# Optimization experiments

Hardware: AMD Instinct MI355X
Metric: run time of the kernel (lower is better)

Reference implementation:

```python
import jax, jax.numpy as jnp
import numpy as np

MAX_SEQ_LEN = 4096

def bigbird_block_rand_mask(from_seq_length, to_seq_length, from_block_size, to_block_size, num_rand_blocks, last_idx=-1):
    rand_attn = np.zeros((from_seq_length // from_block_size - 2, num_rand_blocks), dtype=np.int32)
    middle_seq = np.arange(1, to_seq_length // to_block_size - 1, dtype=np.int32)
    last = to_seq_length // to_block_size - 1
    if last_idx > 2 * to_block_size:
        last = last_idx // to_block_size - 1
    r = num_rand_blocks
    nfb = from_seq_length // from_block_size
    for i in range(1, nfb - 1):
        start = i - 2
        end = i
        if i == 1:
            rand_attn[i - 1, :] = np.random.permutation(middle_seq[2:last])[:r]
        elif i == 2:
            rand_attn[i - 1, :] = np.random.permutation(middle_seq[3:last])[:r]
        elif i == nfb - 3:
            rand_attn[i - 1, :] = np.random.permutation(middle_seq[:last])[:r]
        elif i == nfb - 2:
            rand_attn[i - 1, :] = np.random.permutation(middle_seq[:last])[:r]
        elif start > last:
            start = last
            rand_attn[i - 1, :] = np.random.permutation(middle_seq[:start])[:r]
        elif end + 1 == last:
            rand_attn[i - 1, :] = np.random.permutation(middle_seq[:start])[:r]
        else:
            rand_attn[i - 1, :] = np.random.permutation(np.concatenate((middle_seq[:start], middle_seq[end + 1:last])))[:r]
    return rand_attn

def full_bigbird_mask(from_seq_length, to_seq_length, from_block_size, to_block_size, rand_attn):
    attn_mask = np.zeros((MAX_SEQ_LEN, MAX_SEQ_LEN), dtype=np.int32)
    for i in range(1, from_seq_length // from_block_size - 1):
        attn_mask[i * from_block_size:(i + 1) * from_block_size, (i - 1) * to_block_size:(i + 2) * to_block_size] = 1
        for j in rand_attn[i - 1, :]:
            attn_mask[i * from_block_size:(i + 1) * from_block_size, j * to_block_size:(j + 1) * to_block_size] = 1
    attn_mask[:from_block_size, :] = 1
    attn_mask[:, :to_block_size] = 1
    attn_mask[:, -to_block_size:] = 1
    attn_mask[-from_block_size:, :] = 1
    return attn_mask[:from_seq_length, :to_seq_length].astype(bool)

def setup_inputs() -> dict:
    B, H, F, T, D = 2, 16, 1024, 1024, 64
    BS, R, SEED = 64, 3, 0
    np.random.seed(SEED)
    rand_attn = np.stack([
        bigbird_block_rand_mask(MAX_SEQ_LEN, MAX_SEQ_LEN, BS, BS, R, last_idx=1024)[:F // BS - 2]
        for _ in range(H)
    ], axis=0)
    mask = np.stack([full_bigbird_mask(F, T, BS, BS, rand_attn[h]) for h in range(H)], axis=0)
    attention_mask = jnp.asarray(mask[None].astype(np.float32))  # [1, H, F, T]
    key = jax.random.key(0)
    kq, kk, kv = jax.random.split(key, 3)
    return {
        'query_layer': jax.random.normal(kq, (B, H, F, D), dtype=jnp.float32),
        'key_layer': jax.random.normal(kk, (B, H, T, D), dtype=jnp.float32),
        'value_layer': jax.random.normal(kv, (B, H, T, D), dtype=jnp.float32),
        'attention_mask': attention_mask,
    }

def reference(query_layer, key_layer, value_layer, attention_mask):
    d = query_layer.shape[-1]
    scores = jnp.einsum('bnfh,bnth->bnft', query_layer, key_layer) * (1.0 / np.sqrt(float(d)))
    scores = scores + (1.0 - attention_mask) * -10000.0
    probs = jax.nn.softmax(scores, axis=-1)
    # [batch, from_seq, heads, size_per_head]
    return jnp.einsum('bnft,bnth->bfnh', probs, value_layer)
```

## Files before the change

kernel.cpp:

```cpp
#include <hip/hip_runtime.h>

typedef __attribute__((ext_vector_type(4))) float f32x4;
typedef __attribute__((ext_vector_type(8))) short bf16x8;
typedef _Float16 f16x8 __attribute__((ext_vector_type(8)));

#define MFMA16(a, b, c) __builtin_amdgcn_mfma_f32_16x16x32_f16((a), (b), (c), 0, 0, 0)
#define MFMABF(a, b, c) __builtin_amdgcn_mfma_f32_16x16x32_bf16((a), (b), (c), 0, 0, 0)

constexpr size_t TILE_FRAG_BYTES = 8192;
constexpr size_t NTILES = 512;
constexpr size_t ARR_S  = NTILES * TILE_FRAG_BYTES;
constexpr size_t WS_NEED = 2 * ARR_S;

__device__ __forceinline__ int swz_off(int row, int col) {
    return (row * 128 + col * 2) ^ ((row & 7) << 4);
}
__device__ __forceinline__ f16x8 ld_frag16(const char* tile, int row, int col) {
    return *(const f16x8*)(tile + swz_off(row, col));
}

__global__ __launch_bounds__(256) void bigbird_prepass(
    const float* __restrict__ K, const float* __restrict__ V,
    char* __restrict__ ws) {
    __shared__ float vf[64][66];
    const int tile = blockIdx.x;
    const int tid  = threadIdx.x;
    const float* Kt = K + (size_t)tile * 4096;
    const float* Vt = V + (size_t)tile * 4096;
    f16x8* Ko = (f16x8*)(ws + (size_t)tile * TILE_FRAG_BYTES);
    f16x8* Vo = (f16x8*)(ws + ARR_S + (size_t)tile * TILE_FRAG_BYTES);

    {
        const int row = tid >> 2;
        const int c0  = (tid & 3) << 4;
        const float* p = Vt + row * 64 + c0;
        f32x4 e0 = *(const f32x4*)p,       e1 = *(const f32x4*)(p + 4),
              e2 = *(const f32x4*)(p + 8), e3 = *(const f32x4*)(p + 12);
#pragma unroll
        for (int e = 0; e < 4; ++e) {
            vf[row][c0 + e] = e0[e];     vf[row][c0 + 4 + e] = e1[e];
            vf[row][c0 + 8 + e] = e2[e]; vf[row][c0 + 12 + e] = e3[e];
        }
    }
#pragma unroll
    for (int t = 0; t < 2; ++t) {
        int s = tid + t * 256;
        int f = s >> 6, lane = s & 63;
        int j = f >> 1, kk = f & 1;
        int l16 = lane & 15, g = lane >> 4;
        const float* p = Kt + (j * 16 + l16) * 64 + kk * 32 + g * 8;
        f32x4 a = *(const f32x4*)p;
        f32x4 c = *(const f32x4*)(p + 4);
        f16x8 kv;
#pragma unroll
        for (int e = 0; e < 4; ++e) {
            kv[e]     = (_Float16)a[e];
            kv[4 + e] = (_Float16)c[e];
        }
        Ko[s] = kv;
    }
    __syncthreads();
#pragma unroll
    for (int t = 0; t < 2; ++t) {
        int s = tid + t * 256;
        int f = s >> 6, lane = s & 63;
        int j = f >> 1, kk = f & 1;
        int l16 = lane & 15, g = lane >> 4;
        f16x8 vv;
#pragma unroll
        for (int e = 0; e < 8; ++e)
            vv[e] = (_Float16)vf[kk * 32 + g * 8 + e][j * 16 + l16];
        Vo[s] = vv;
    }
}

__global__ __launch_bounds__(256) void bigbird_main(
    const float* __restrict__ Q, const float* __restrict__ M,
    const char* __restrict__ ws, float* __restrict__ Out) {
    constexpr int H = 16, F = 1024, D = 64;

    __shared__ char p_sm[4][2048];
    __shared__ int flags[16];
    __shared__ int list[16];
    __shared__ int ncnt;

    const int i0  = blockIdx.x;
    const int xcd = i0 & 7;
    const int q0  = i0 >> 3;
    const int grp = xcd * 4 + (q0 >> 4);
    const int fb  = q0 & 15;
    const int b   = grp >> 4;
    const int h   = grp & 15;
    const int bh  = grp;

    const int tid  = threadIdx.x;
    const int lane = tid & 63;
    const int w    = tid >> 6;
    const int g    = lane >> 4;
    const int l16  = lane & 15;

    if (tid < 16)
        flags[tid] = (M[((size_t)(h * 1024 + fb * 64)) * 1024 + tid * 64] > 0.5f) ? 1 : 0;

    f16x8 qf[2];
    {
        const float* qr = Q + ((size_t)bh * F + fb * 64 + w * 16 + l16) * D;
#pragma unroll
        for (int kk = 0; kk < 2; ++kk) {
            const float* p = qr + kk * 32 + g * 8;
            f32x4 a = *(const f32x4*)p;
            f32x4 c = *(const f32x4*)(p + 4);
#pragma unroll
            for (int e = 0; e < 8; ++e)
                qf[kk][e] = (_Float16)((e < 4 ? a[e] : c[e - 4]) * 0.125f);
        }
    }
    __syncthreads();
    if (tid == 0) {
        int nn = 0;
        for (int t = 0; t < 16; ++t)
            if (flags[t]) list[nn++] = t;
        ncnt = nn;
    }
    __syncthreads();
    const int n = ncnt;

    const f16x8* Kbase = (const f16x8*)ws + (size_t)bh * 16 * 512;
    const f16x8* Vbase = (const f16x8*)(ws + ARR_S) + (size_t)bh * 16 * 512;
    char* pw = p_sm[w];

    float mrow[4];
#pragma unroll
    for (int r = 0; r < 4; ++r) mrow[r] = -1e30f;

    for (int i = 0; i < n; ++i) {
        const f16x8* Kf = Kbase + (size_t)list[i] * 512;
        f16x8 kfr[4][2];
#pragma unroll
        for (int j = 0; j < 4; ++j)
#pragma unroll
            for (int kk = 0; kk < 2; ++kk)
                kfr[j][kk] = Kf[(j * 2 + kk) * 64 + lane];
        f32x4 sv[4];
#pragma unroll
        for (int j = 0; j < 4; ++j) {
            sv[j] = f32x4{0.f, 0.f, 0.f, 0.f};
#pragma unroll
            for (int kk = 0; kk < 2; ++kk)
                sv[j] = MFMA16(qf[kk], kfr[j][kk], sv[j]);
        }
#pragma unroll
        for (int r = 0; r < 4; ++r)
            mrow[r] = fmaxf(mrow[r],
                      fmaxf(fmaxf(sv[0][r], sv[1][r]), fmaxf(sv[2][r], sv[3][r])));
    }
#pragma unroll
    for (int off = 1; off < 16; off <<= 1)
#pragma unroll
        for (int r = 0; r < 4; ++r)
            mrow[r] = fmaxf(mrow[r], __shfl_xor(mrow[r], off, 64));

    f32x4 acc[4];
    float lsum[4];
#pragma unroll
    for (int j = 0; j < 4; ++j) acc[j] = f32x4{0.f, 0.f, 0.f, 0.f};
#pragma unroll
    for (int r = 0; r < 4; ++r) lsum[r] = 0.f;

    for (int i = 0; i < n; ++i) {
        const int tb = list[i];
        const f16x8* Kf = Kbase + (size_t)tb * 512;
        const f16x8* Vf = Vbase + (size_t)tb * 512;
        f16x8 kfr[4][2], vfr[4][2];
#pragma unroll
        for (int j = 0; j < 4; ++j)
#pragma unroll
            for (int kk = 0; kk < 2; ++kk) {
                kfr[j][kk] = Kf[(j * 2 + kk) * 64 + lane];
                vfr[j][kk] = Vf[(j * 2 + kk) * 64 + lane];
            }
        f32x4 sv[4];
#pragma unroll
        for (int j = 0; j < 4; ++j) {
            sv[j] = f32x4{0.f, 0.f, 0.f, 0.f};
#pragma unroll
            for (int kk = 0; kk < 2; ++kk)
                sv[j] = MFMA16(qf[kk], kfr[j][kk], sv[j]);
        }
#pragma unroll
        for (int j = 0; j < 4; ++j)
#pragma unroll
            for (int r = 0; r < 4; ++r) {
                float pe = __expf(sv[j][r] - mrow[r]);
                sv[j][r] = pe;
                lsum[r] += pe;
            }
#pragma unroll
        for (int j = 0; j < 4; ++j)
#pragma unroll
            for (int r = 0; r < 4; ++r)
                *(_Float16*)(pw + swz_off(g * 4 + r, j * 16 + l16)) = (_Float16)sv[j][r];
        asm volatile("s_waitcnt lgkmcnt(0)" ::: "memory");
        __builtin_amdgcn_sched_barrier(0);
#pragma unroll
        for (int kk = 0; kk < 2; ++kk) {
            f16x8 pa = ld_frag16(pw, l16, kk * 32 + g * 8);
#pragma unroll
            for (int jd = 0; jd < 4; ++jd)
                acc[jd] = MFMA16(pa, vfr[jd][kk], acc[jd]);
        }
    }

#pragma unroll
    for (int off = 1; off < 16; off <<= 1)
#pragma unroll
        for (int r = 0; r < 4; ++r)
            lsum[r] += __shfl_xor(lsum[r], off, 64);

#pragma unroll
    for (int r = 0; r < 4; ++r) {
        float inv = 1.0f / lsum[r];
        int f = fb * 64 + w * 16 + g * 4 + r;
        float* ob = Out + ((size_t)(b * F + f) * H + h) * D;
#pragma unroll
        for (int jd = 0; jd < 4; ++jd)
            ob[jd * 16 + l16] = acc[jd][r] * inv;
    }
}

__device__ __forceinline__ unsigned short f2bf(float x) {
    unsigned u = __builtin_bit_cast(unsigned, x);
    unsigned r = u + 0x7fffu + ((u >> 16) & 1u);
    return (unsigned short)(r >> 16);
}
__device__ __forceinline__ float bf2f(unsigned short h) {
    return __builtin_bit_cast(float, (unsigned)h << 16);
}
__device__ __forceinline__ bf16x8 ld_fragb(const char* tile, int row, int col) {
    return *(const bf16x8*)(tile + swz_off(row, col));
}
__device__ __forceinline__ void stage_rm_fb(const float* __restrict__ src,
                                            char* hi_t, char* lo_t, float scale) {
    const int tid = threadIdx.x;
    const int row = tid >> 2;
    const int c0  = (tid & 3) << 4;
    const float* p = src + row * 64 + c0;
    f32x4 vv[4] = { *(const f32x4*)(p), *(const f32x4*)(p + 4),
                    *(const f32x4*)(p + 8), *(const f32x4*)(p + 12) };
    bf16x8 h2[2], l2[2];
#pragma unroll
    for (int e = 0; e < 16; ++e) {
        float x = vv[e >> 2][e & 3] * scale;
        unsigned short hb = f2bf(x);
        unsigned short lb = f2bf(x - bf2f(hb));
        h2[e >> 3][e & 7] = (short)hb;
        l2[e >> 3][e & 7] = (short)lb;
    }
#pragma unroll
    for (int gi = 0; gi < 2; ++gi) {
        int off = swz_off(row, c0 + gi * 8);
        *(bf16x8*)(hi_t + off) = h2[gi];
        *(bf16x8*)(lo_t + off) = l2[gi];
    }
}
__device__ __forceinline__ void stage_tr_fb(const float* __restrict__ src,
                                            char* hi_t, char* lo_t) {
    const int tid = threadIdx.x;
    const int t  = tid >> 2;
    const int c0 = (tid & 3) << 4;
    const float* p = src + t * 64 + c0;
    f32x4 vv[4] = { *(const f32x4*)(p), *(const f32x4*)(p + 4),
                    *(const f32x4*)(p + 8), *(const f32x4*)(p + 12) };
#pragma unroll
    for (int e = 0; e < 16; ++e) {
        float x = vv[e >> 2][e & 3];
        unsigned short hb = f2bf(x);
        unsigned short lb = f2bf(x - bf2f(hb));
        int d = c0 + e;
        int off = (d * 128 + t * 2) ^ ((d & 7) << 4);
        *(unsigned short*)(hi_t + off) = hb;
        *(unsigned short*)(lo_t + off) = lb;
    }
}
__global__ __launch_bounds__(256) void bigbird_kernel_fb(
    const float* __restrict__ Q, const float* __restrict__ K,
    const float* __restrict__ V, const float* __restrict__ M,
    float* __restrict__ Out) {
    constexpr int H = 16, F = 1024, D = 64;
    __shared__ char kq_hi[8192];
    __shared__ char kq_lo[8192];
    __shared__ char vt_hi[8192];
    __shared__ char vt_lo[8192];
    __shared__ char p_smf[8192];
    __shared__ int flags[16];
    const int bid = blockIdx.x;
    const int fb  = bid & 15;
    const int h   = (bid >> 4) & 15;
    const int b   = bid >> 8;
    const int tid  = threadIdx.x;
    const int lane = tid & 63;
    const int w    = tid >> 6;
    const int g    = lane >> 4;
    const int l16  = lane & 15;
    if (tid < 16)
        flags[tid] = (M[(h * 1024 + fb * 64) * 1024 + tid * 64] > 0.5f) ? 1 : 0;
    const float* qb = Q + ((size_t)(b * H + h) * F + fb * 64) * D;
    stage_rm_fb(qb, kq_hi, kq_lo, 0.125f);
    __syncthreads();
    bf16x8 qh[2], ql[2];
#pragma unroll
    for (int kk = 0; kk < 2; ++kk) {
        qh[kk] = ld_fragb(kq_hi, w * 16 + l16, kk * 32 + g * 8);
        ql[kk] = ld_fragb(kq_lo, w * 16 + l16, kk * 32 + g * 8);
    }
    f32x4 acc[4];
    float m_r[4], l_r[4];
#pragma unroll
    for (int j = 0; j < 4; ++j) acc[j] = f32x4{0.f, 0.f, 0.f, 0.f};
#pragma unroll
    for (int r = 0; r < 4; ++r) { m_r[r] = -1e30f; l_r[r] = 0.f; }
    const float* kb = K + (size_t)(b * H + h) * 1024 * D;
    const float* vb = V + (size_t)(b * H + h) * 1024 * D;
    for (int tb = 0; tb < 16; ++tb) {
        if (!flags[tb]) continue;
        __syncthreads();
        stage_rm_fb(kb + tb * 64 * D, kq_hi, kq_lo, 1.0f);
        stage_tr_fb(vb + tb * 64 * D, vt_hi, vt_lo);
        __syncthreads();
        f32x4 s[4];
#pragma unroll
        for (int j = 0; j < 4; ++j) {
            s[j] = f32x4{0.f, 0.f, 0.f, 0.f};
#pragma unroll
            for (int kk = 0; kk < 2; ++kk) {
                bf16x8 bhf = ld_fragb(kq_hi, j * 16 + l16, kk * 32 + g * 8);
                bf16x8 blf = ld_fragb(kq_lo, j * 16 + l16, kk * 32 + g * 8);
                s[j] = MFMABF(qh[kk], bhf, s[j]);
                s[j] = MFMABF(qh[kk], blf, s[j]);
                s[j] = MFMABF(ql[kk], bhf, s[j]);
            }
        }
        float rmax[4];
#pragma unroll
        for (int r = 0; r < 4; ++r)
            rmax[r] = fmaxf(fmaxf(s[0][r], s[1][r]), fmaxf(s[2][r], s[3][r]));
#pragma unroll
        for (int off = 1; off < 16; off <<= 1)
#pragma unroll
            for (int r = 0; r < 4; ++r)
                rmax[r] = fmaxf(rmax[r], __shfl_xor(rmax[r], off, 64));
        float alpha[4], psum[4];
#pragma unroll
        for (int r = 0; r < 4; ++r) {
            float mn = fmaxf(m_r[r], rmax[r]);
            alpha[r] = __expf(m_r[r] - mn);
            m_r[r]   = mn;
            psum[r]  = 0.f;
        }
#pragma unroll
        for (int j = 0; j < 4; ++j)
#pragma unroll
            for (int r = 0; r < 4; ++r) {
                float pe = __expf(s[j][r] - m_r[r]);
                s[j][r] = pe;
                psum[r] += pe;
            }
#pragma unroll
        for (int off = 1; off < 16; off <<= 1)
#pragma unroll
            for (int r = 0; r < 4; ++r)
                psum[r] += __shfl_xor(psum[r], off, 64);
#pragma unroll
        for (int r = 0; r < 4; ++r)
            l_r[r] = l_r[r] * alpha[r] + psum[r];
#pragma unroll
        for (int j = 0; j < 4; ++j)
#pragma unroll
            for (int r = 0; r < 4; ++r)
                acc[j][r] *= alpha[r];
#pragma unroll
        for (int j = 0; j < 4; ++j)
#pragma unroll
            for (int r = 0; r < 4; ++r) {
                int row = w * 16 + g * 4 + r;
                *(unsigned short*)(p_smf + swz_off(row, j * 16 + l16)) = f2bf(s[j][r]);
            }
        __syncthreads();
#pragma unroll
        for (int kk = 0; kk < 2; ++kk) {
            bf16x8 pa = ld_fragb(p_smf, w * 16 + l16, kk * 32 + g * 8);
#pragma unroll
            for (int jd = 0; jd < 4; ++jd) {
                bf16x8 vh = ld_fragb(vt_hi, jd * 16 + l16, kk * 32 + g * 8);
                bf16x8 vl = ld_fragb(vt_lo, jd * 16 + l16, kk * 32 + g * 8);
                acc[jd] = MFMABF(pa, vh, acc[jd]);
                acc[jd] = MFMABF(pa, vl, acc[jd]);
            }
        }
    }
#pragma unroll
    for (int r = 0; r < 4; ++r) {
        float inv = 1.0f / l_r[r];
        int f = fb * 64 + w * 16 + g * 4 + r;
        float* ob = Out + ((size_t)(b * F + f) * H + h) * D;
#pragma unroll
        for (int jd = 0; jd < 4; ++jd)
            ob[jd * 16 + l16] = acc[jd][r] * inv;
    }
}

extern "C" void kernel_launch(void* const* d_in, const int* in_sizes, int n_in,
                              void* d_out, int out_size, void* d_ws, size_t ws_size,
                              hipStream_t stream) {
    const float* q = (const float*)d_in[0];
    const float* k = (const float*)d_in[1];
    const float* v = (const float*)d_in[2];
    const float* m = (const float*)d_in[3];
    float* out = (float*)d_out;
    if (ws_size >= WS_NEED) {
        bigbird_prepass<<<dim3(512), dim3(256), 0, stream>>>(k, v, (char*)d_ws);
        bigbird_main<<<dim3(512), dim3(256), 0, stream>>>(q, m, (const char*)d_ws, out);
    } else {
        bigbird_kernel_fb<<<dim3(512), dim3(256), 0, stream>>>(q, k, v, m, out);
    }
}
```

Measured before the change: 41.60 us.

## Split key blocks across waves with split-K softmax merge in LDS

```diff
diff --git a/kernel.cpp b/kernel.cpp
--- a/kernel.cpp
+++ b/kernel.cpp
@@ -79,19 +79,18 @@
     const char* __restrict__ ws, float* __restrict__ Out) {
     constexpr int H = 16, F = 1024, D = 64;
 
-    __shared__ char p_sm[4][2048];
+    __shared__ char  p_sm[4][8192];
+    __shared__ float O_sm[64][65];
+    __shared__ float m_sm[4][64], l_sm[4][64];
     __shared__ int flags[16];
     __shared__ int list[16];
     __shared__ int ncnt;
 
-    const int i0  = blockIdx.x;
-    const int xcd = i0 & 7;
-    const int q0  = i0 >> 3;
-    const int grp = xcd * 4 + (q0 >> 4);
-    const int fb  = q0 & 15;
-    const int b   = grp >> 4;
-    const int h   = grp & 15;
-    const int bh  = grp;
+    const int bid = blockIdx.x;
+    const int bh  = bid >> 4;
+    const int fb  = bid & 15;
+    const int b   = bh >> 4;
+    const int h   = bh & 15;
 
     const int tid  = threadIdx.x;
     const int lane = tid & 63;
@@ -102,9 +101,10 @@
     if (tid < 16)
         flags[tid] = (M[((size_t)(h * 1024 + fb * 64)) * 1024 + tid * 64] > 0.5f) ? 1 : 0;
 
-    f16x8 qf[2];
-    {
-        const float* qr = Q + ((size_t)bh * F + fb * 64 + w * 16 + l16) * D;
+    f16x8 qf[4][2];
+#pragma unroll
+    for (int jr = 0; jr < 4; ++jr) {
+        const float* qr = Q + ((size_t)bh * F + fb * 64 + jr * 16 + l16) * D;
 #pragma unroll
         for (int kk = 0; kk < 2; ++kk) {
             const float* p = qr + kk * 32 + g * 8;
@@ -112,7 +112,7 @@
             f32x4 c = *(const f32x4*)(p + 4);
 #pragma unroll
             for (int e = 0; e < 8; ++e)
-                qf[kk][e] = (_Float16)((e < 4 ? a[e] : c[e - 4]) * 0.125f);
+                qf[jr][kk][e] = (_Float16)((e < 4 ? a[e] : c[e - 4]) * 0.125f);
         }
     }
     __syncthreads();
@@ -129,102 +129,166 @@
     const f16x8* Vbase = (const f16x8*)(ws + ARR_S) + (size_t)bh * 16 * 512;
     char* pw = p_sm[w];
 
-    float mrow[4];
-#pragma unroll
-    for (int r = 0; r < 4; ++r) mrow[r] = -1e30f;
-
-    for (int i = 0; i < n; ++i) {
+    float mrow[4][4];
+#pragma unroll
+    for (int jr = 0; jr < 4; ++jr)
+#pragma unroll
+        for (int r = 0; r < 4; ++r) mrow[jr][r] = -1e30f;
+
+    for (int i = w; i < n; i += 4) {
         const f16x8* Kf = Kbase + (size_t)list[i] * 512;
         f16x8 kfr[4][2];
 #pragma unroll
-        for (int j = 0; j < 4; ++j)
+        for (int jc = 0; jc < 4; ++jc)
 #pragma unroll
             for (int kk = 0; kk < 2; ++kk)
-                kfr[j][kk] = Kf[(j * 2 + kk) * 64 + lane];
-        f32x4 sv[4];
-#pragma unroll
-        for (int j = 0; j < 4; ++j) {
-            sv[j] = f32x4{0.f, 0.f, 0.f, 0.f};
-#pragma unroll
-            for (int kk = 0; kk < 2; ++kk)
-                sv[j] = MFMA16(qf[kk], kfr[j][kk], sv[j]);
-        }
-#pragma unroll
-        for (int r = 0; r < 4; ++r)
-            mrow[r] = fmaxf(mrow[r],
-                      fmaxf(fmaxf(sv[0][r], sv[1][r]), fmaxf(sv[2][r], sv[3][r])));
+                kfr[jc][kk] = Kf[(jc * 2 + kk) * 64 + lane];
+#pragma unroll
+        for (int jc = 0; jc < 4; ++jc) {
+#pragma unroll
+            for (int jr = 0; jr < 4; ++jr) {
+                f32x4 s = f32x4{0.f, 0.f, 0.f, 0.f};
+#pragma unroll
+                for (int kk = 0; kk < 2; ++kk)
+                    s = MFMA16(qf[jr][kk], kfr[jc][kk], s);
+#pragma unroll
+                for (int r = 0; r < 4; ++r)
+                    mrow[jr][r] = fmaxf(mrow[jr][r], s[r]);
+            }
+        }
     }
 #pragma unroll
     for (int off = 1; off < 16; off <<= 1)
 #pragma unroll
-        for (int r = 0; r < 4; ++r)
-            mrow[r] = fmaxf(mrow[r], __shfl_xor(mrow[r], off, 64));
-
-    f32x4 acc[4];
-    float lsum[4];
-#pragma unroll
-    for (int j = 0; j < 4; ++j) acc[j] = f32x4{0.f, 0.f, 0.f, 0.f};
-#pragma unroll
-    for (int r = 0; r < 4; ++r) lsum[r] = 0.f;
-
-    for (int i = 0; i < n; ++i) {
+        for (int jr = 0; jr < 4; ++jr)
+#pragma unroll
+            for (int r = 0; r < 4; ++r)
+                mrow[jr][r] = fmaxf(mrow[jr][r], __shfl_xor(mrow[jr][r], off, 64));
+
+    f32x4 acc[4][4];
+    float lsum[4][4];
+#pragma unroll
+    for (int jr = 0; jr < 4; ++jr)
+#pragma unroll
+        for (int jd = 0; jd < 4; ++jd) acc[jr][jd] = f32x4{0.f, 0.f, 0.f, 0.f};
+#pragma unroll
+    for (int jr = 0; jr < 4; ++jr)
+#pragma unroll
+        for (int r = 0; r < 4; ++r) lsum[jr][r] = 0.f;
+
+    for (int i = w; i < n; i += 4) {
         const int tb = list[i];
         const f16x8* Kf = Kbase + (size_t)tb * 512;
         const f16x8* Vf = Vbase + (size_t)tb * 512;
-        f16x8 kfr[4][2], vfr[4][2];
-#pragma unroll
-        for (int j = 0; j < 4; ++j)
-#pragma unroll
-            for (int kk = 0; kk < 2; ++kk) {
-                kfr[j][kk] = Kf[(j * 2 + kk) * 64 + lane];
-                vfr[j][kk] = Vf[(j * 2 + kk) * 64 + lane];
-            }
-        f32x4 sv[4];
-#pragma unroll
-        for (int j = 0; j < 4; ++j) {
-            sv[j] = f32x4{0.f, 0.f, 0.f, 0.f};
-#pragma unroll
-            for (int kk = 0; kk < 2; ++kk)
-                sv[j] = MFMA16(qf[kk], kfr[j][kk], sv[j]);
-        }
-#pragma unroll
-        for (int j = 0; j < 4; ++j)
-#pragma unroll
-            for (int r = 0; r < 4; ++r) {
-                float pe = __expf(sv[j][r] - mrow[r]);
-                sv[j][r] = pe;
-                lsum[r] += pe;
-            }
-#pragma unroll
-        for (int j = 0; j < 4; ++j)
-#pragma unroll
-            for (int r = 0; r < 4; ++r)
-                *(_Float16*)(pw + swz_off(g * 4 + r, j * 16 + l16)) = (_Float16)sv[j][r];
+        {
+            f16x8 kfr[4][2];
+#pragma unroll
+            for (int jc = 0; jc < 4; ++jc)
+#pragma unroll
+                for (int kk = 0; kk < 2; ++kk)
+                    kfr[jc][kk] = Kf[(jc * 2 + kk) * 64 + lane];
+#pragma unroll
+            for (int jc = 0; jc < 4; ++jc) {
+#pragma unroll
+                for (int jr = 0; jr < 4; ++jr) {
+                    f32x4 s = f32x4{0.f, 0.f, 0.f, 0.f};
+#pragma unroll
+                    for (int kk = 0; kk < 2; ++kk)
+                        s = MFMA16(qf[jr][kk], kfr[jc][kk], s);
+#pragma unroll
+                    for (int r = 0; r < 4; ++r) {
+                        float pe = __expf(s[r] - mrow[jr][r]);
+                        lsum[jr][r] += pe;
+                        *(_Float16*)(pw + swz_off(jr * 16 + g * 4 + r,
+                                                  jc * 16 + l16)) = (_Float16)pe;
+                    }
+                }
+            }
+        }
         asm volatile("s_waitcnt lgkmcnt(0)" ::: "memory");
         __builtin_amdgcn_sched_barrier(0);
-#pragma unroll
-        for (int kk = 0; kk < 2; ++kk) {
-            f16x8 pa = ld_frag16(pw, l16, kk * 32 + g * 8);
+        {
+            f16x8 vfr[4][2];
 #pragma unroll
             for (int jd = 0; jd < 4; ++jd)
-                acc[jd] = MFMA16(pa, vfr[jd][kk], acc[jd]);
+#pragma unroll
+                for (int kk = 0; kk < 2; ++kk)
+                    vfr[jd][kk] = Vf[(jd * 2 + kk) * 64 + lane];
+#pragma unroll
+            for (int kk = 0; kk < 2; ++kk)
+#pragma unroll
+                for (int jr = 0; jr < 4; ++jr) {
+                    f16x8 pa = ld_frag16(pw, jr * 16 + l16, kk * 32 + g * 8);
+#pragma unroll
+                    for (int jd = 0; jd < 4; ++jd)
+                        acc[jr][jd] = MFMA16(pa, vfr[jd][kk], acc[jr][jd]);
+                }
         }
     }
 
 #pragma unroll
     for (int off = 1; off < 16; off <<= 1)
 #pragma unroll
-        for (int r = 0; r < 4; ++r)
-            lsum[r] += __shfl_xor(lsum[r], off, 64);
-
-#pragma unroll
-    for (int r = 0; r < 4; ++r) {
-        float inv = 1.0f / lsum[r];
-        int f = fb * 64 + w * 16 + g * 4 + r;
-        float* ob = Out + ((size_t)(b * F + f) * H + h) * D;
-#pragma unroll
-        for (int jd = 0; jd < 4; ++jd)
-            ob[jd * 16 + l16] = acc[jd][r] * inv;
+        for (int jr = 0; jr < 4; ++jr)
+#pragma unroll
+            for (int r = 0; r < 4; ++r)
+                lsum[jr][r] += __shfl_xor(lsum[jr][r], off, 64);
+
+    if (l16 == 0) {
+#pragma unroll
+        for (int jr = 0; jr < 4; ++jr)
+#pragma unroll
+            for (int r = 0; r < 4; ++r) {
+                int row = jr * 16 + g * 4 + r;
+                m_sm[w][row] = mrow[jr][r];
+                l_sm[w][row] = lsum[jr][r];
+            }
+    }
+    __syncthreads();
+    float wgt[4][4];
+#pragma unroll
+    for (int jr = 0; jr < 4; ++jr)
+#pragma unroll
+        for (int r = 0; r < 4; ++r) {
+            int row = jr * 16 + g * 4 + r;
+            float Mx = fmaxf(fmaxf(m_sm[0][row], m_sm[1][row]),
+                             fmaxf(m_sm[2][row], m_sm[3][row]));
+            wgt[jr][r] = __expf(mrow[jr][r] - Mx);
+        }
+#pragma unroll
+    for (int ww = 0; ww < 4; ++ww) {
+        if (w == ww) {
+#pragma unroll
+            for (int jr = 0; jr < 4; ++jr)
+#pragma unroll
+                for (int jd = 0; jd < 4; ++jd)
+#pragma unroll
+                    for (int r = 0; r < 4; ++r) {
+                        int row = jr * 16 + g * 4 + r;
+                        int col = jd * 16 + l16;
+                        float v = acc[jr][jd][r] * wgt[jr][r];
+                        if (ww == 0) O_sm[row][col] = v;
+                        else         O_sm[row][col] += v;
+                    }
+        }
+        __syncthreads();
+    }
+
+    {
+        const int row = tid >> 2;
+        const int q4  = tid & 3;
+        float Mx = fmaxf(fmaxf(m_sm[0][row], m_sm[1][row]),
+                         fmaxf(m_sm[2][row], m_sm[3][row]));
+        float L = 0.f;
+#pragma unroll
+        for (int ww = 0; ww < 4; ++ww)
+            L += l_sm[ww][row] * __expf(m_sm[ww][row] - Mx);
+        float inv = 1.0f / L;
+        int f = fb * 64 + row;
+        float* ob = Out + ((size_t)(b * F + f) * H + h) * D + q4 * 16;
+#pragma unroll
+        for (int e = 0; e < 16; ++e)
+            ob[e] = O_sm[row][q4 * 16 + e] * inv;
     }
 }
 
```

Measured after the change: 65.13 us. +56.6%, slower.
